# Kernel optimization log

Measured on AMD Instinct MI355X. Metric: run time of the kernel, lower is better.

Reference implementation:

```python
import jax, jax.numpy as jnp
import numpy as np

EPSILON = 0.1
NSTEPS = 2
SIGN = 1.0  # forward integration (sample direction)


def setup_inputs() -> dict:
    key = jax.random.key(0)
    ks = jax.random.split(key, 6)
    B, D, H = 4096, 32, 256
    x = jax.random.normal(ks[0], (B, D), jnp.float32)
    logp = jax.random.normal(ks[1], (B,), jnp.float32)
    w1 = jax.random.normal(ks[2], (D, H), jnp.float32) / np.sqrt(D).astype(np.float32)
    b1 = jax.random.normal(ks[3], (H,), jnp.float32) * 0.01
    w2 = jax.random.normal(ks[4], (H,), jnp.float32) / np.sqrt(H).astype(np.float32)
    b2 = jax.random.normal(ks[5], (1,), jnp.float32) * 0.01
    return {"x": x, "logp": logp, "w1": w1, "b1": b1, "w2": w2, "b2": b2}


def reference(x, logp, w1, b1, w2, b2):
    D = x.shape[-1]

    def u(xi):  # scalar Brenier potential for a single sample [D] -> scalar
        h = jax.nn.softplus(xi @ w1 + b1)
        return h @ w2 + b2[0]

    grad_u = jax.grad(u)  # net.grad: du/dx, [D] -> [D]

    def lap_u(xi):  # net.laplacian: trace of Hessian via forward-over-reverse HVPs
        eye = jnp.eye(D, dtype=xi.dtype)
        hvp = lambda v: jax.jvp(grad_u, (xi,), (v,))[1]
        return jnp.trace(jax.vmap(hvp)(eye))

    v_grad = jax.vmap(grad_u)   # [B,D] -> [B,D]
    v_lap = jax.vmap(lap_u)     # [B,D] -> [B]

    def ode(xc):
        return SIGN * EPSILON * v_grad(xc), -SIGN * EPSILON * v_lap(xc)

    def step(carry, _):
        xc, lp = carry
        k1x, k1l = ode(xc)
        k2x, k2l = ode(xc + k1x / 2)
        k3x, k3l = ode(xc + k2x / 2)
        k4x, k4l = ode(xc + k3x)
        xc = xc + (k1x / 6.0 + k2x / 3.0 + k3x / 3.0 + k4x / 6.0)
        lp = lp + (k1l / 6.0 + k2l / 3.0 + k3l / 3.0 + k4l / 6.0)
        return (xc, lp), None

    (x, logp), _ = jax.lax.scan(step, (x, logp), None, length=NSTEPS)
    return x, logp
```

## Files before the change

### kernel.cpp

```cpp
#include <hip/hip_runtime.h>

#define B_TOTAL 4096
#define D 32
#define H 256
#define SPB 16
#define NW 8
#define HPW 32
#define PGS 34
#define XCS 40

static constexpr float EPS = 0.1f;

typedef __attribute__((ext_vector_type(8))) short short8v;
typedef __attribute__((ext_vector_type(4))) float f32x4;

__device__ __forceinline__ unsigned short bf16rne(float f) {
  unsigned u = __float_as_uint(f);
  u += 0x7FFFu + ((u >> 16) & 1u);
  return (unsigned short)(u >> 16);
}
__device__ __forceinline__ float fromb(unsigned short h) {
  return __uint_as_float(((unsigned)h) << 16);
}
__device__ __forceinline__ void split_rne(float f, unsigned short& hi, unsigned short& lo) {
  hi = bf16rne(f); lo = bf16rne(f - fromb(hi));
}

#define MFMA16(A, Bf, C) __builtin_amdgcn_mfma_f32_16x16x32_bf16((A), (Bf), (C), 0, 0, 0)


__global__ __launch_bounds__(512, 2) void ma_flow_kernel(
    const float* __restrict__ x_in, const float* __restrict__ logp_in,
    const float* __restrict__ w1, const float* __restrict__ b1,
    const float* __restrict__ w2, float* __restrict__ out)
{
  __shared__ __align__(16) float partG[NW][SPB][PGS];
  __shared__ __align__(16) unsigned short xcH[SPB][XCS];
  __shared__ __align__(16) unsigned short xcL[SPB][XCS];

  const int tid = threadIdx.x;
  const int l  = tid & 63;
  const int wv = tid >> 6;
  const int lr = l & 15;
  const int lg = l >> 4;
  const int hbase = wv * HPW;
  const int s_own = tid >> 5;
  const int d_own = tid & 31;
  const int xci = ((d_own & 15) << 1) | (d_own >> 4);

  short8v Bzh[2], Bzl[2];
  float ctau[2];
#pragma unroll
  for (int tau = 0; tau < 2; ++tau) {
    const int h = hbase + tau * 16 + lr;
    float cpart = 0.0f;
    short8v hi, lo;
#pragma unroll
    for (int j = 0; j < 8; ++j) {
      const int dj = lg * 4 + (j >> 1) + ((j & 1) << 4);
      float w = w1[dj * H + h];
      cpart = fmaf(w, w, cpart);
      unsigned short hb, lb; split_rne(w, hb, lb);
      hi[j] = (short)hb; lo[j] = (short)lb;
    }
    Bzh[tau] = hi; Bzl[tau] = lo;
    cpart += __shfl_xor(cpart, 16);
    cpart += __shfl_xor(cpart, 32);
    ctau[tau] = cpart;
  }
  f32x4 b1v[2], w2v[2], w2cv[2];
#pragma unroll
  for (int tau = 0; tau < 2; ++tau)
#pragma unroll
    for (int r = 0; r < 4; ++r) {
      const int hh = hbase + tau * 16 + lg * 4 + r;
      b1v[tau][r] = b1[hh];
      float w2x = w2[hh];
      w2v[tau][r] = w2x;
      w2cv[tau][r] = w2x * __shfl(ctau[tau], lg * 4 + r);
    }
  short8v Bgh[2], Bgl[2];
#pragma unroll
  for (int nu = 0; nu < 2; ++nu) {
    const int d = nu * 16 + lr;
    short8v hi, lo;
#pragma unroll
    for (int j = 0; j < 8; ++j) {
      const int hl = ((j >> 2) << 4) + lg * 4 + (j & 3);
      float w = w1[d * H + hbase + hl];
      unsigned short hb, lb; split_rne(w, hb, lb);
      hi[j] = (short)hb; lo[j] = (short)lb;
    }
    Bgh[nu] = hi; Bgl[nu] = lo;
  }

  float x0r = x_in[blockIdx.x * (SPB * D) + tid];
  float accr = 0.0f;
  {
    unsigned u = __float_as_uint(x0r);
    xcH[s_own][xci] = (unsigned short)(u >> 16);
    float res = x0r - __uint_as_float(u & 0xFFFF0000u);
    xcL[s_own][xci] = (unsigned short)(__float_as_uint(res) >> 16);
  }
  float lp = (tid < SPB) ? logp_in[blockIdx.x * SPB + tid] : 0.0f;
  float lapAcc = 0.0f;
  __syncthreads();

#pragma unroll 1
  for (int stage = 0; stage < 8; ++stage) {
    const int st = stage & 3;
    const float wa = (st == 0 || st == 3) ? (EPS / 6.0f) : (EPS / 3.0f);
    const float wc = (st == 2) ? EPS : (EPS * 0.5f);

    short8v xh = *reinterpret_cast<const short8v*>(&xcH[lr][lg * 8]);
    short8v xl = *reinterpret_cast<const short8v*>(&xcL[lr][lg * 8]);

    f32x4 zz[2];
#pragma unroll
    for (int tau = 0; tau < 2; ++tau) {
      f32x4 z = MFMA16(Bzh[tau], xh, b1v[tau]);
      z = MFMA16(Bzh[tau], xl, z);
      z = MFMA16(Bzl[tau], xh, z);
      zz[tau] = z;
    }
    float q = 0.0f;
    unsigned short ab[2][4];
#pragma unroll
    for (int tau = 0; tau < 2; ++tau)
#pragma unroll
      for (int r = 0; r < 4; ++r) {
        float E = __expf(-zz[tau][r]);
        float t = __builtin_amdgcn_rcpf(1.0f + E);
        q = fmaf(t * t * E, w2cv[tau][r], q);
        ab[tau][r] = bf16rne(t * w2v[tau][r]);
      }
    lapAcc = fmaf(wa, q, lapAcc);
    short8v aF;
#pragma unroll
    for (int j = 0; j < 8; ++j) aF[j] = (short)ab[j >> 2][j & 3];

#pragma unroll
    for (int nu = 0; nu < 2; ++nu) {
      f32x4 g = {0.0f, 0.0f, 0.0f, 0.0f};
      g = MFMA16(aF, Bgh[nu], g);
      g = MFMA16(aF, Bgl[nu], g);
#pragma unroll
      for (int r = 0; r < 4; ++r)
        partG[wv][lg * 4 + r][nu * 16 + lr] = g[r];
    }
    __syncthreads();

    float p0 = partG[0][s_own][d_own], p1 = partG[1][s_own][d_own];
    float p2 = partG[2][s_own][d_own], p3 = partG[3][s_own][d_own];
    float p4 = partG[4][s_own][d_own], p5 = partG[5][s_own][d_own];
    float p6 = partG[6][s_own][d_own], p7 = partG[7][s_own][d_own];
    float gsum = ((p0 + p1) + (p2 + p3)) + ((p4 + p5) + (p6 + p7));
    accr = fmaf(wa, gsum, accr);
    float xw;
    if (st < 3) {
      xw = fmaf(wc, gsum, x0r);
    } else {
      x0r += accr; accr = 0.0f; xw = x0r;
    }
    {
      unsigned u = __float_as_uint(xw);
      xcH[s_own][xci] = (unsigned short)(u >> 16);
      float res = xw - __uint_as_float(u & 0xFFFF0000u);
      xcL[s_own][xci] = (unsigned short)(__float_as_uint(res) >> 16);
    }
    __syncthreads();
  }

  lapAcc += __shfl_xor(lapAcc, 16);
  lapAcc += __shfl_xor(lapAcc, 32);
  if (l < 16) partG[wv][lr][0] = lapAcc;
  __syncthreads();

  out[blockIdx.x * (SPB * D) + tid] = x0r;
  if (tid < SPB) {
    float lt = 0.0f;
#pragma unroll
    for (int w = 0; w < NW; ++w) lt += partG[w][tid][0];
    out[B_TOTAL * D + blockIdx.x * SPB + tid] = lp - lt;
  }
}

extern "C" void kernel_launch(void* const* d_in, const int* in_sizes, int n_in,
                              void* d_out, int out_size, void* d_ws, size_t ws_size,
                              hipStream_t stream) {
  const float* x    = (const float*)d_in[0];
  const float* logp = (const float*)d_in[1];
  const float* w1   = (const float*)d_in[2];
  const float* b1   = (const float*)d_in[3];
  const float* w2   = (const float*)d_in[4];
  float* out = (float*)d_out;

  ma_flow_kernel<<<B_TOTAL / SPB, 512, 0, stream>>>(x, logp, w1, b1, w2, out);
}
```

Baseline: 14.38 us.

## Split hidden dimension across 16 waves with 1024-thread blocks

New measurement: 15.24 us. +6.0%, slower.

```diff
diff --git a/kernel.cpp b/kernel.cpp
--- a/kernel.cpp
+++ b/kernel.cpp
@@ -4,8 +4,8 @@
 #define D 32
 #define H 256
 #define SPB 16
-#define NW 8
-#define HPW 32
+#define NW 16
+#define HPW 16
 #define PGS 34
 #define XCS 40
 
@@ -29,7 +29,7 @@
 #define MFMA16(A, Bf, C) __builtin_amdgcn_mfma_f32_16x16x32_bf16((A), (Bf), (C), 0, 0, 0)
 
 
-__global__ __launch_bounds__(512, 2) void ma_flow_kernel(
+__global__ __launch_bounds__(1024, 4) void ma_flow_kernel(
     const float* __restrict__ x_in, const float* __restrict__ logp_in,
     const float* __restrict__ w1, const float* __restrict__ b1,
     const float* __restrict__ w2, float* __restrict__ out)
@@ -48,37 +48,31 @@
   const int d_own = tid & 31;
   const int xci = ((d_own & 15) << 1) | (d_own >> 4);
 
-  short8v Bzh[2], Bzl[2];
-  float ctau[2];
-#pragma unroll
-  for (int tau = 0; tau < 2; ++tau) {
-    const int h = hbase + tau * 16 + lr;
-    float cpart = 0.0f;
+  short8v Bzh, Bzl;
+  float cpart = 0.0f;
+  {
     short8v hi, lo;
 #pragma unroll
     for (int j = 0; j < 8; ++j) {
       const int dj = lg * 4 + (j >> 1) + ((j & 1) << 4);
-      float w = w1[dj * H + h];
+      float w = w1[dj * H + hbase + lr];
       cpart = fmaf(w, w, cpart);
       unsigned short hb, lb; split_rne(w, hb, lb);
       hi[j] = (short)hb; lo[j] = (short)lb;
     }
-    Bzh[tau] = hi; Bzl[tau] = lo;
+    Bzh = hi; Bzl = lo;
     cpart += __shfl_xor(cpart, 16);
     cpart += __shfl_xor(cpart, 32);
-    ctau[tau] = cpart;
   }
-  f32x4 b1v[2], w2v[2], w2cv[2];
+  f32x4 b1v, w2v, w2cv;
 #pragma unroll
-  for (int tau = 0; tau < 2; ++tau)
-#pragma unroll
-    for (int r = 0; r < 4; ++r) {
-      const int hh = hbase + tau * 16 + lg * 4 + r;
-      b1v[tau][r] = b1[hh];
-      float w2x = w2[hh];
-      w2v[tau][r] = w2x;
-      w2cv[tau][r] = w2x * __shfl(ctau[tau], lg * 4 + r);
-    }
+  for (int r = 0; r < 4; ++r) {
+    const int hh = hbase + lg * 4 + r;
+    b1v[r] = b1[hh];
+    float w2x = w2[hh];
+    w2v[r] = w2x;
+    w2cv[r] = w2x * __shfl(cpart, lg * 4 + r);
+  }
   short8v Bgh[2], Bgl[2];
 #pragma unroll
   for (int nu = 0; nu < 2; ++nu) {
@@ -86,23 +80,26 @@
     short8v hi, lo;
 #pragma unroll
     for (int j = 0; j < 8; ++j) {
-      const int hl = ((j >> 2) << 4) + lg * 4 + (j & 3);
-      float w = w1[d * H + hbase + hl];
-      unsigned short hb, lb; split_rne(w, hb, lb);
-      hi[j] = (short)hb; lo[j] = (short)lb;
+      if (j < 4) {
+        float w = w1[d * H + hbase + lg * 4 + j];
+        unsigned short hb, lb; split_rne(w, hb, lb);
+        hi[j] = (short)hb; lo[j] = (short)lb;
+      } else {
+        hi[j] = 0; lo[j] = 0;
+      }
     }
     Bgh[nu] = hi; Bgl[nu] = lo;
   }
 
-  float x0r = x_in[blockIdx.x * (SPB * D) + tid];
-  float accr = 0.0f;
-  {
+  float x0r = 0.0f, accr = 0.0f, lp = 0.0f;
+  if (tid < SPB * D) {
+    x0r = x_in[blockIdx.x * (SPB * D) + tid];
     unsigned u = __float_as_uint(x0r);
     xcH[s_own][xci] = (unsigned short)(u >> 16);
     float res = x0r - __uint_as_float(u & 0xFFFF0000u);
     xcL[s_own][xci] = (unsigned short)(__float_as_uint(res) >> 16);
   }
-  float lp = (tid < SPB) ? logp_in[blockIdx.x * SPB + tid] : 0.0f;
+  if (tid < SPB) lp = logp_in[blockIdx.x * SPB + tid];
   float lapAcc = 0.0f;
   __syncthreads();
 
@@ -115,29 +112,23 @@
     short8v xh = *reinterpret_cast<const short8v*>(&xcH[lr][lg * 8]);
     short8v xl = *reinterpret_cast<const short8v*>(&xcL[lr][lg * 8]);
 
-    f32x4 zz[2];
+    f32x4 z = MFMA16(Bzh, xh, b1v);
+    z = MFMA16(Bzh, xl, z);
+    z = MFMA16(Bzl, xh, z);
+
+    float q = 0.0f;
+    unsigned short ab[4];
 #pragma unroll
-    for (int tau = 0; tau < 2; ++tau) {
-      f32x4 z = MFMA16(Bzh[tau], xh, b1v[tau]);
-      z = MFMA16(Bzh[tau], xl, z);
-      z = MFMA16(Bzl[tau], xh, z);
-      zz[tau] = z;
+    for (int r = 0; r < 4; ++r) {
+      float E = __expf(-z[r]);
+      float t = __builtin_amdgcn_rcpf(1.0f + E);
+      q = fmaf(t * t * E, w2cv[r], q);
+      ab[r] = bf16rne(t * w2v[r]);
     }
-    float q = 0.0f;
-    unsigned short ab[2][4];
-#pragma unroll
-    for (int tau = 0; tau < 2; ++tau)
-#pragma unroll
-      for (int r = 0; r < 4; ++r) {
-        float E = __expf(-zz[tau][r]);
-        float t = __builtin_amdgcn_rcpf(1.0f + E);
-        q = fmaf(t * t * E, w2cv[tau][r], q);
-        ab[tau][r] = bf16rne(t * w2v[tau][r]);
-      }
     lapAcc = fmaf(wa, q, lapAcc);
     short8v aF;
 #pragma unroll
-    for (int j = 0; j < 8; ++j) aF[j] = (short)ab[j >> 2][j & 3];
+    for (int j = 0; j < 8; ++j) aF[j] = (j < 4) ? (short)ab[j] : (short)0;
 
 #pragma unroll
     for (int nu = 0; nu < 2; ++nu) {
@@ -150,19 +141,19 @@
     }
     __syncthreads();
 
-    float p0 = partG[0][s_own][d_own], p1 = partG[1][s_own][d_own];
-    float p2 = partG[2][s_own][d_own], p3 = partG[3][s_own][d_own];
-    float p4 = partG[4][s_own][d_own], p5 = partG[5][s_own][d_own];
-    float p6 = partG[6][s_own][d_own], p7 = partG[7][s_own][d_own];
-    float gsum = ((p0 + p1) + (p2 + p3)) + ((p4 + p5) + (p6 + p7));
-    accr = fmaf(wa, gsum, accr);
-    float xw;
-    if (st < 3) {
-      xw = fmaf(wc, gsum, x0r);
-    } else {
-      x0r += accr; accr = 0.0f; xw = x0r;
-    }
-    {
+    if (tid < SPB * D) {
+      float ps[NW];
+#pragma unroll
+      for (int w = 0; w < NW; ++w) ps[w] = partG[w][s_own][d_own];
+      float gsum = (((ps[0] + ps[1]) + (ps[2] + ps[3])) + ((ps[4] + ps[5]) + (ps[6] + ps[7])))
+                 + (((ps[8] + ps[9]) + (ps[10] + ps[11])) + ((ps[12] + ps[13]) + (ps[14] + ps[15])));
+      accr = fmaf(wa, gsum, accr);
+      float xw;
+      if (st < 3) {
+        xw = fmaf(wc, gsum, x0r);
+      } else {
+        x0r += accr; accr = 0.0f; xw = x0r;
+      }
       unsigned u = __float_as_uint(xw);
       xcH[s_own][xci] = (unsigned short)(u >> 16);
       float res = xw - __uint_as_float(u & 0xFFFF0000u);
@@ -176,7 +167,7 @@
   if (l < 16) partG[wv][lr][0] = lapAcc;
   __syncthreads();
 
-  out[blockIdx.x * (SPB * D) + tid] = x0r;
+  if (tid < SPB * D) out[blockIdx.x * (SPB * D) + tid] = x0r;
   if (tid < SPB) {
     float lt = 0.0f;
 #pragma unroll
@@ -195,5 +186,5 @@
   const float* w2   = (const float*)d_in[4];
   float* out = (float*)d_out;
 
-  ma_flow_kernel<<<B_TOTAL / SPB, 512, 0, stream>>>(x, logp, w1, b1, w2, out);
+  ma_flow_kernel<<<B_TOTAL / SPB, 1024, 0, stream>>>(x, logp, w1, b1, w2, out);
 }
```

## Reduce gradient partials via LDS atomics into triple-buffered accumulator, drop second barrier

Applied to the files above, without the earlier changes.

Result: slower. 55.16 us (+283.6%).

```diff
diff --git a/kernel.cpp b/kernel.cpp
--- a/kernel.cpp
+++ b/kernel.cpp
@@ -6,8 +6,7 @@
 #define SPB 16
 #define NW 8
 #define HPW 32
-#define PGS 34
-#define XCS 40
+#define GAS 36
 
 static constexpr float EPS = 0.1f;
 
@@ -34,9 +33,8 @@
     const float* __restrict__ w1, const float* __restrict__ b1,
     const float* __restrict__ w2, float* __restrict__ out)
 {
-  __shared__ __align__(16) float partG[NW][SPB][PGS];
-  __shared__ __align__(16) unsigned short xcH[SPB][XCS];
-  __shared__ __align__(16) unsigned short xcL[SPB][XCS];
+  __shared__ __align__(16) float gAcc[3][SPB][GAS];
+  __shared__ float lapB[NW][SPB];
 
   const int tid = threadIdx.x;
   const int l  = tid & 63;
@@ -44,9 +42,6 @@
   const int lr = l & 15;
   const int lg = l >> 4;
   const int hbase = wv * HPW;
-  const int s_own = tid >> 5;
-  const int d_own = tid & 31;
-  const int xci = ((d_own & 15) << 1) | (d_own >> 4);
 
   short8v Bzh[2], Bzl[2];
   float ctau[2];
@@ -94,26 +89,43 @@
     Bgh[nu] = hi; Bgl[nu] = lo;
   }
 
-  float x0r = x_in[blockIdx.x * (SPB * D) + tid];
-  float accr = 0.0f;
+  for (int i = tid; i < SPB * GAS; i += 512) gAcc[0][0][i] = 0.0f;
   {
-    unsigned u = __float_as_uint(x0r);
-    xcH[s_own][xci] = (unsigned short)(u >> 16);
-    float res = x0r - __uint_as_float(u & 0xFFFF0000u);
-    xcL[s_own][xci] = (unsigned short)(__float_as_uint(res) >> 16);
-  }
-  float lp = (tid < SPB) ? logp_in[blockIdx.x * SPB + tid] : 0.0f;
+    float xv = x_in[blockIdx.x * (SPB * D) + tid];
+    int s = tid >> 5, d = tid & 31;
+    gAcc[2][s][((d & 15) << 1) | (d >> 4)] = xv;
+  }
+  __syncthreads();
+
+  float x0r[8], accr[8];
+  short8v xh, xl;
+  {
+    const float* xp = &gAcc[2][lr][lg * 8];
+    f32x4 xa = *reinterpret_cast<const f32x4*>(xp);
+    f32x4 xb = *reinterpret_cast<const f32x4*>(xp + 4);
+    float xv8[8] = {xa.x, xa.y, xa.z, xa.w, xb.x, xb.y, xb.z, xb.w};
+#pragma unroll
+    for (int j = 0; j < 8; ++j) {
+      x0r[j] = xv8[j]; accr[j] = 0.0f;
+      unsigned u = __float_as_uint(xv8[j]);
+      xh[j] = (short)(u >> 16);
+      xl[j] = (short)(__float_as_uint(xv8[j] - __uint_as_float(u & 0xFFFF0000u)) >> 16);
+    }
+  }
   float lapAcc = 0.0f;
-  __syncthreads();
 
 #pragma unroll 1
   for (int stage = 0; stage < 8; ++stage) {
     const int st = stage & 3;
     const float wa = (st == 0 || st == 3) ? (EPS / 6.0f) : (EPS / 3.0f);
     const float wc = (st == 2) ? EPS : (EPS * 0.5f);
-
-    short8v xh = *reinterpret_cast<const short8v*>(&xcH[lr][lg * 8]);
-    short8v xl = *reinterpret_cast<const short8v*>(&xcL[lr][lg * 8]);
+    const int cb = stage % 3;
+    const int nb = (stage + 1) % 3;
+
+    {
+      float* zb = &gAcc[nb][0][0];
+      for (int i = tid; i < SPB * GAS; i += 512) zb[i] = 0.0f;
+    }
 
     f32x4 zz[2];
 #pragma unroll
@@ -146,42 +158,46 @@
       g = MFMA16(aF, Bgl[nu], g);
 #pragma unroll
       for (int r = 0; r < 4; ++r)
-        partG[wv][lg * 4 + r][nu * 16 + lr] = g[r];
+        atomicAdd(&gAcc[cb][lg * 4 + r][2 * lr + nu], g[r]);
     }
     __syncthreads();
 
-    float p0 = partG[0][s_own][d_own], p1 = partG[1][s_own][d_own];
-    float p2 = partG[2][s_own][d_own], p3 = partG[3][s_own][d_own];
-    float p4 = partG[4][s_own][d_own], p5 = partG[5][s_own][d_own];
-    float p6 = partG[6][s_own][d_own], p7 = partG[7][s_own][d_own];
-    float gsum = ((p0 + p1) + (p2 + p3)) + ((p4 + p5) + (p6 + p7));
-    accr = fmaf(wa, gsum, accr);
-    float xw;
-    if (st < 3) {
-      xw = fmaf(wc, gsum, x0r);
-    } else {
-      x0r += accr; accr = 0.0f; xw = x0r;
-    }
-    {
+    const float* gp = &gAcc[cb][lr][lg * 8];
+    f32x4 ga = *reinterpret_cast<const f32x4*>(gp);
+    f32x4 gb = *reinterpret_cast<const f32x4*>(gp + 4);
+    float gv[8] = {ga.x, ga.y, ga.z, ga.w, gb.x, gb.y, gb.z, gb.w};
+#pragma unroll
+    for (int j = 0; j < 8; ++j) {
+      accr[j] = fmaf(wa, gv[j], accr[j]);
+      float xw;
+      if (st < 3) {
+        xw = fmaf(wc, gv[j], x0r[j]);
+      } else {
+        x0r[j] += accr[j]; accr[j] = 0.0f; xw = x0r[j];
+      }
       unsigned u = __float_as_uint(xw);
-      xcH[s_own][xci] = (unsigned short)(u >> 16);
-      float res = xw - __uint_as_float(u & 0xFFFF0000u);
-      xcL[s_own][xci] = (unsigned short)(__float_as_uint(res) >> 16);
-    }
-    __syncthreads();
+      xh[j] = (short)(u >> 16);
+      xl[j] = (short)(__float_as_uint(xw - __uint_as_float(u & 0xFFFF0000u)) >> 16);
+    }
   }
 
   lapAcc += __shfl_xor(lapAcc, 16);
   lapAcc += __shfl_xor(lapAcc, 32);
-  if (l < 16) partG[wv][lr][0] = lapAcc;
+  if (l < 16) lapB[wv][lr] = lapAcc;
   __syncthreads();
 
-  out[blockIdx.x * (SPB * D) + tid] = x0r;
+  {
+    float vout = x0r[0];
+#pragma unroll
+    for (int j = 1; j < 8; ++j) if (wv == j) vout = x0r[j];
+    const int dslot = lg * 4 + (wv >> 1) + ((wv & 1) << 4);
+    out[(blockIdx.x * SPB + lr) * D + dslot] = vout;
+  }
   if (tid < SPB) {
     float lt = 0.0f;
 #pragma unroll
-    for (int w = 0; w < NW; ++w) lt += partG[w][tid][0];
-    out[B_TOTAL * D + blockIdx.x * SPB + tid] = lp - lt;
+    for (int w = 0; w < NW; ++w) lt += lapB[w][tid];
+    out[B_TOTAL * D + blockIdx.x * SPB + tid] = logp_in[blockIdx.x * SPB + tid] - lt;
   }
 }
 
```
